# Kernel optimization log

Hardware: AMD Instinct MI355X
Metric: run time of the kernel (lower is better)

## Reference

```python
import jax, jax.numpy as jnp
import numpy as np

S, D, H, A_EMB = 128, 128, 512, 32   # memory_slots, memory_dim, integrator_hidden_dim, action_embedding_dim
FRAME_D = 512
NUM_ACTIONS = 12
T = 8192


def setup_inputs() -> dict:
    key = jax.random.key(0)
    ks = jax.random.split(key, 16)
    def rn(k, shape, scale=0.02):
        return jax.random.normal(k, shape, dtype=jnp.float32) * scale
    concat = FRAME_D + D + A_EMB
    return {
        "frame_embeds": jax.random.normal(ks[0], (T, FRAME_D), dtype=jnp.float32),
        "actions": jax.random.randint(ks[1], (T,), 0, NUM_ACTIONS),
        "action_embed_table": rn(ks[2], (NUM_ACTIONS + 1, A_EMB)),
        "W_ih": rn(ks[3], (4 * H, concat)),
        "W_hh": rn(ks[4], (4 * H, H)),
        "b_ih": jnp.zeros((4 * H,), jnp.float32),
        "b_hh": jnp.zeros((4 * H,), jnp.float32),
        "W_cls": rn(ks[5], (NUM_ACTIONS, H)),
        "b_cls": jnp.zeros((NUM_ACTIONS,), jnp.float32),
        "memory_init": rn(ks[6], (S, D)),
        "Wq": rn(ks[7], (D, H)), "bq": jnp.zeros((D,), jnp.float32),
        "Wk": rn(ks[8], (D, D)), "bk": jnp.zeros((D,), jnp.float32),
        "Wv": rn(ks[9], (D, D)), "bv": jnp.zeros((D,), jnp.float32),
        "Ww": rn(ks[10], (D, H)), "bw": jnp.zeros((D,), jnp.float32),
        "wg": rn(ks[11], (1, H)), "bg": jnp.zeros((1,), jnp.float32),
    }


def reference(frame_embeds, actions, action_embed_table, W_ih, W_hh, b_ih, b_hh,
              W_cls, b_cls, memory_init, Wq, bq, Wk, bk, Wv, bv, Ww, bw, wg, bg):
    T_ = frame_embeds.shape[0]
    # prev_actions = [start_action_index] + actions[:-1]
    prev_actions = jnp.concatenate([jnp.full((1,), NUM_ACTIONS, actions.dtype), actions[:-1]])
    prev_emb = action_embed_table[prev_actions]          # [T, A_EMB]
    keys0 = memory_init @ Wk.T + bk                      # [S, D]
    vals0 = memory_init @ Wv.T + bv                      # [S, D]
    h0 = jnp.zeros((H,), frame_embeds.dtype)
    c0 = jnp.zeros((H,), frame_embeds.dtype)
    scale = 1.0 / np.sqrt(D).astype(np.float32)

    def step(carry, xs):
        h, c, keys, vals = carry
        fe, pe, is_first = xs
        # soft memory read (skipped on step 0: retrieved = 0, and no write that step)
        q = h @ Wq.T + bq                                # [D]
        attn = jax.nn.softmax(keys @ q * scale)          # [S]
        mask = 1.0 - is_first
        retrieved = mask * (attn @ vals)                 # [D]
        x = jnp.concatenate([fe, retrieved, pe])         # [concat]
        # torch LSTMCell: gate order i, f, g, o
        gates = x @ W_ih.T + b_ih + h @ W_hh.T + b_hh    # [4H]
        i, f, g, o = jnp.split(gates, 4)
        c_new = jax.nn.sigmoid(f) * c + jax.nn.sigmoid(i) * jnp.tanh(g)
        h_new = jax.nn.sigmoid(o) * jnp.tanh(c_new)
        # gated memory write using this step's attention
        gate = jax.nn.sigmoid(h_new @ wg.T + bg)[0]      # scalar
        write_vec = h_new @ Ww.T + bw                    # [D]
        w = (mask * gate * attn)[:, None]                # [S, 1]
        vals_new = vals * (1.0 - w) + w * write_vec
        keys_new = keys * (1.0 - w) + w * write_vec
        logit = h_new @ W_cls.T + b_cls                  # [num_actions] (dropout eval = identity)
        return (h_new, c_new, keys_new, vals_new), logit

    is_first = jnp.zeros((T_,), frame_embeds.dtype).at[0].set(1.0)
    _, logits = jax.lax.scan(step, (h0, c0, keys0, vals0), (frame_embeds, prev_emb, is_first))
    return logits  # [T, num_actions]
```

## Files before the change

kernel.cpp:

```cpp
#include <hip/hip_runtime.h>

#define NGWG 128
#define TSTEPS 8192

typedef unsigned int u32;
typedef unsigned long long u64;

__device__ __forceinline__ u32 rne16(float f) {
    u32 u = __float_as_uint(f);
    return (u + 0x7fffu + ((u >> 16) & 1u)) >> 16;
}
__device__ __forceinline__ u32 packbf(float a, float b) {
    return rne16(a) | (rne16(b) << 16);
}
__device__ __forceinline__ float bflo(u32 u) { return __uint_as_float(u << 16); }
__device__ __forceinline__ float bfhi(u32 u) { return __uint_as_float(u & 0xffff0000u); }

#if __has_builtin(__builtin_amdgcn_fdot2_f32_bf16)
typedef __bf16 bf16x2 __attribute__((ext_vector_type(2)));
__device__ __forceinline__ float dot2b(u32 w, u32 h, float acc) {
    return __builtin_amdgcn_fdot2_f32_bf16(__builtin_bit_cast(bf16x2, w),
                                           __builtin_bit_cast(bf16x2, h), acc, false);
}
#else
__device__ __forceinline__ float dot2b(u32 w, u32 h, float acc) {
    return acc + bflo(w) * bflo(h) + bfhi(w) * bfhi(h);
}
#endif

__device__ __forceinline__ float rsum64(float a) {
#pragma unroll
    for (int m = 1; m < 64; m <<= 1) a += __shfl_xor(a, m);
    return a;
}
__device__ __forceinline__ float sigm(float x) { return 1.f / (1.f + __expf(-x)); }

template <typename PT>
__global__ __launch_bounds__(256) void k_pre(const float* __restrict__ fe,
                                             const int* __restrict__ act,
                                             const float* __restrict__ aet,
                                             const float* __restrict__ wih,
                                             const float* __restrict__ bih,
                                             const float* __restrict__ bhh,
                                             PT* __restrict__ P) {
    __shared__ __align__(16) float xs[32][68];
    __shared__ int pa[32];
    const int b = blockIdx.x;
    const int t0 = (b >> 3) * 32;
    const int jb = b & 7;
    const int tid = threadIdx.x;
    const int j = jb * 256 + tid;
    float acc[32];
#pragma unroll
    for (int i = 0; i < 32; i++) acc[i] = 0.f;
    if (tid < 32) {
        int t = t0 + tid;
        pa[tid] = (t == 0) ? 12 : act[t - 1];
    }
    const float* wrow = wih + (size_t)j * 672;
    for (int c = 0; c < 8; c++) {
        __syncthreads();
        for (int i = tid; i < 32 * 68; i += 256) {
            int tl = i / 68, kk = i % 68;
            int kg = c * 68 + kk;
            float v = (kg < 512) ? fe[(size_t)(t0 + tl) * 512 + kg]
                                 : aet[pa[tl] * 32 + (kg - 512)];
            xs[tl][kk] = v;
        }
        __syncthreads();
#pragma unroll
        for (int m = 0; m < 17; m++) {
            int kg0 = c * 68 + 4 * m;
            int col = (kg0 < 512) ? kg0 : kg0 + 128;
            float4 w = *(const float4*)(wrow + col);
#pragma unroll
            for (int tl = 0; tl < 32; tl++) {
                float4 x = *(const float4*)(&xs[tl][4 * m]);
                acc[tl] += w.x * x.x + w.y * x.y + w.z * x.z + w.w * x.w;
            }
        }
    }
    float bias = bih[j] + bhh[j];
    int jq = j >> 9, jrem = j & 511, jg = jrem >> 2, ju = jrem & 3;
#pragma unroll 4
    for (int tl = 0; tl < 32; tl++) {
        size_t idx = ((size_t)(t0 + tl) * NGWG + jg) * 16 + 4 * jq + ju;
        float v = acc[tl] + bias;
        if constexpr (sizeof(PT) == 2) P[idx] = (PT)rne16(v);
        else P[idx] = v;
    }
}

__global__ __launch_bounds__(256) void k_kv(const float* __restrict__ mi,
                                            const float* __restrict__ wk,
                                            const float* __restrict__ bk,
                                            const float* __restrict__ wv,
                                            const float* __restrict__ bv,
                                            float* __restrict__ kv0) {
    int o = blockIdx.x * 256 + threadIdx.x;
    int which = o >> 14;
    int rest = o & 16383;
    int s = rest >> 7, d = rest & 127;
    const float* W = which ? wv : wk;
    float acc = which ? bv[d] : bk[d];
    const float* mrow = mi + s * 128;
    const float* wrow = W + d * 128;
#pragma unroll
    for (int k = 0; k < 128; k += 4) {
        float4 a = *(const float4*)(mrow + k);
        float4 b2 = *(const float4*)(wrow + k);
        acc += a.x * b2.x + a.y * b2.y + a.z * b2.z + a.w * b2.w;
    }
    kv0[o] = acc;
}

template <typename PT>
__global__ __launch_bounds__(1024) void k_seq(const PT* __restrict__ P,
                                              const float* __restrict__ kv0,
                                              u64* __restrict__ hw,
                                              const float* __restrict__ Whh,
                                              const float* __restrict__ Wih,
                                              const float* __restrict__ Wq,
                                              const float* __restrict__ bq,
                                              const float* __restrict__ Ww,
                                              const float* __restrict__ bw,
                                              const float* __restrict__ wg,
                                              const float* __restrict__ bg,
                                              const float* __restrict__ Wcls,
                                              const float* __restrict__ bcls,
                                              float* __restrict__ out) {
    __shared__ __align__(16) float hfp[512];
    __shared__ __align__(16) u32 hbf[256];
    __shared__ __align__(16) float qwv[256];
    __shared__ float biasq[256];
    __shared__ float attn[128];
    __shared__ float warr[128];
    __shared__ float scr[128];
    __shared__ __align__(16) float part[1024];
    __shared__ float gats[16];
    __shared__ float retr[128];
    __shared__ float wgld[512];
    __shared__ float misc[4];

    const int tid = threadIdx.x;
    const int lane = tid & 63;
    const int wave = tid >> 6;
    const int g = blockIdx.x;

    if (g == NGWG) {
        float wc[8];
        float bc = 0.f;
        if (wave < 12) {
#pragma unroll
            for (int i = 0; i < 8; i++) wc[i] = Wcls[wave * 512 + 8 * lane + i];
            bc = bcls[wave];
        }
        for (int t = 0; t < TSTEPS; ++t) {
            if (tid < 512) {
                const u64* p = hw + ((size_t)((t + 1) & 3)) * 512 + tid;
                u64 v;
                do {
                    v = __hip_atomic_load(p, __ATOMIC_RELAXED, __HIP_MEMORY_SCOPE_AGENT);
                } while ((u32)(v >> 32) != (u32)(t + 1));
                hfp[tid] = __uint_as_float((u32)v);
            }
            __syncthreads();
            if (wave < 12) {
                float a = 0.f;
#pragma unroll
                for (int i = 0; i < 8; i++) a += wc[i] * hfp[8 * lane + i];
                a = rsum64(a);
                if (lane == 0) out[t * 12 + wave] = a + bc;
            }
            __syncthreads();
        }
        return;
    }

    const int seg = tid >> 8;
    const int o = tid & 255;
    const int s = tid >> 3;
    const int dc = tid & 7;
    const int dv = tid >> 3;
    const int s8 = tid & 7;

    u32 whhp[4], wirp;
    {
        int r = wave;
        int row = ((r >> 2) << 9) + 4 * g + (r & 3);
        const float* wr = Whh + (size_t)row * 512 + 8 * lane;
        float4 a = *(const float4*)wr;
        float4 b2 = *(const float4*)(wr + 4);
        whhp[0] = packbf(a.x, a.y);
        whhp[1] = packbf(a.z, a.w);
        whhp[2] = packbf(b2.x, b2.y);
        whhp[3] = packbf(b2.z, b2.w);
        const float* ir = Wih + (size_t)row * 672 + 512 + 2 * lane;
        wirp = packbf(ir[0], ir[1]);
    }
    u32 wqw[64];
    {
        const float* src = ((o < 128) ? (Wq + (size_t)o * 512) : (Ww + (size_t)(o - 128) * 512)) + seg * 128;
#pragma unroll
        for (int i = 0; i < 32; i++) {
            float4 v = *(const float4*)(src + 4 * i);
            wqw[2 * i] = packbf(v.x, v.y);
            wqw[2 * i + 1] = packbf(v.z, v.w);
        }
    }
    float keys[16], valsT[16];
    {
        const float* kp = kv0 + s * 128 + 16 * dc;
#pragma unroll
        for (int i = 0; i < 16; i++) keys[i] = kp[i];
#pragma unroll
        for (int i = 0; i < 16; i++) valsT[i] = kv0[16384 + (16 * s8 + i) * 128 + dv];
    }
    float cst = 0.f;
    const float bg0 = bg[0];

    if (tid < 512) { hfp[tid] = 0.f; wgld[tid] = wg[tid]; }
    if (tid < 256) { hbf[tid] = 0u; biasq[tid] = (tid < 128) ? bq[tid] : bw[tid - 128]; }
    if (tid < 128) { attn[tid] = 0.f; warr[tid] = 0.f; }
    if (tid < 4) misc[tid] = 0.f;
    __syncthreads();

    const float SCALE = 0.08838834764831845f;

    for (int t = 0; t < TSTEPS; ++t) {
        float pv;
        {
            size_t pidx = ((size_t)t * NGWG + g) * 16 + wave;
            if constexpr (sizeof(PT) == 2) pv = __uint_as_float(((u32)P[pidx]) << 16);
            else pv = P[pidx];
        }
        if (t > 0) {
            if (tid < 512) {
                const u64* p = hw + ((size_t)(t & 3)) * 512 + tid;
                u64 v;
                do {
                    v = __hip_atomic_load(p, __ATOMIC_RELAXED, __HIP_MEMORY_SCOPE_AGENT);
                } while ((u32)(v >> 32) != (u32)t);
                float vf = __uint_as_float((u32)v);
                hfp[tid] = vf;
                float other = __shfl_xor(vf, 1);
                if ((tid & 1) == 0) hbf[tid >> 1] = packbf(vf, other);
            }
            __syncthreads();
        }
        {
            const uint4* hb = ((const uint4*)hbf) + (seg << 4);
            float a0 = 0.f, a1 = 0.f;
#pragma unroll
            for (int i = 0; i < 16; i += 2) {
                uint4 x = hb[i];
                uint4 y = hb[i + 1];
                a0 = dot2b(wqw[4 * i + 0], x.x, a0);
                a0 = dot2b(wqw[4 * i + 1], x.y, a0);
                a0 = dot2b(wqw[4 * i + 2], x.z, a0);
                a0 = dot2b(wqw[4 * i + 3], x.w, a0);
                a1 = dot2b(wqw[4 * i + 4], y.x, a1);
                a1 = dot2b(wqw[4 * i + 5], y.y, a1);
                a1 = dot2b(wqw[4 * i + 6], y.z, a1);
                a1 = dot2b(wqw[4 * i + 7], y.w, a1);
            }
            part[tid] = a0 + a1;
        }
        if (wave == 15) {
            float a = 0.f;
#pragma unroll
            for (int i = 0; i < 8; i++) a += wgld[8 * lane + i] * hfp[8 * lane + i];
            a = rsum64(a);
            if (lane == 0) misc[0] = sigm(a + bg0);
        }
        __syncthreads();
        if (tid < 256)
            qwv[tid] = part[tid] + part[tid + 256] + part[tid + 512] + part[tid + 768] + biasq[tid];
        __syncthreads();
        {
            const float* qq = qwv + 16 * dc;
            float a = 0.f;
#pragma unroll
            for (int i = 0; i < 16; i++) a += keys[i] * qq[i];
            a += __shfl_xor(a, 1);
            a += __shfl_xor(a, 2);
            a += __shfl_xor(a, 4);
            if (dc == 0) scr[s] = a;
        }
        __syncthreads();
        if (wave == 0) {
            float a = qwv[lane] * qwv[128 + lane] + qwv[64 + lane] * qwv[192 + lane];
            float wvq = rsum64(a);
            float wmask = (t >= 2) ? 1.f : 0.f;
            float mret = (t > 0) ? 1.f : 0.f;
            float gp = misc[0];
            float w0 = wmask * gp * attn[lane];
            float w1 = wmask * gp * attn[64 + lane];
            float s0 = (scr[lane] * (1.f - w0) + w0 * wvq) * SCALE;
            float s1 = (scr[64 + lane] * (1.f - w1) + w1 * wvq) * SCALE;
            float m = fmaxf(s0, s1);
#pragma unroll
            for (int k = 1; k < 64; k <<= 1) m = fmaxf(m, __shfl_xor(m, k));
            float e0 = __expf(s0 - m), e1 = __expf(s1 - m);
            float su = rsum64(e0 + e1);
            float inv = 1.f / su;
            float a0 = e0 * inv, a1 = e1 * inv;
            attn[lane] = a0;
            attn[64 + lane] = a1;
            warr[lane] = w0;
            warr[64 + lane] = w1;
            scr[lane] = a0 * (1.f - w0) * mret;
            scr[64 + lane] = a1 * (1.f - w1) * mret;
            float bp = rsum64(a0 * w0 + a1 * w1);
            if (lane == 0) misc[2] = bp * mret;
        }
        __syncthreads();
        {
            float a = 0.f;
            const float* ap = scr + 16 * s8;
#pragma unroll
            for (int i = 0; i < 16; i++) a += ap[i] * valsT[i];
            a += __shfl_xor(a, 1);
            a += __shfl_xor(a, 2);
            a += __shfl_xor(a, 4);
            if (s8 == 0) retr[dv] = a + misc[2] * qwv[128 + dv];
        }
        __syncthreads();
        {
            const float* hh = hfp + 8 * lane;
            float a = 0.f;
#pragma unroll
            for (int i = 0; i < 4; i++) {
                u32 u = whhp[i];
                a += bflo(u) * hh[2 * i] + bfhi(u) * hh[2 * i + 1];
            }
            const float* rr = retr + 2 * lane;
            a += bflo(wirp) * rr[0] + bfhi(wirp) * rr[1];
            a = rsum64(a);
            if (lane == 0) gats[wave] = a + pv;
        }
        __syncthreads();
        if (tid < 4) {
            float gi = gats[tid], gf = gats[4 + tid], gg2 = gats[8 + tid], go = gats[12 + tid];
            cst = sigm(gf) * cst + sigm(gi) * tanhf(gg2);
            float hn = sigm(go) * tanhf(cst);
            u64 wv64 = ((u64)(u32)(t + 1) << 32) | (u64)__float_as_uint(hn);
            __hip_atomic_store(hw + ((size_t)((t + 1) & 3)) * 512 + 4 * g + tid, wv64,
                               __ATOMIC_RELAXED, __HIP_MEMORY_SCOPE_AGENT);
        }
        if (t >= 2) {
            float w = warr[s];
            const float* wvp = qwv + 128 + 16 * dc;
#pragma unroll
            for (int i = 0; i < 16; i++) keys[i] += w * (wvp[i] - keys[i]);
            float wvd = qwv[128 + dv];
#pragma unroll
            for (int i = 0; i < 16; i++) {
                float wj = warr[16 * s8 + i];
                valsT[i] += wj * (wvd - valsT[i]);
            }
        }
    }
}

extern "C" void kernel_launch(void* const* d_in, const int* in_sizes, int n_in,
                              void* d_out, int out_size, void* d_ws, size_t ws_size,
                              hipStream_t stream) {
    const float* fe = (const float*)d_in[0];
    const int* act = (const int*)d_in[1];
    const float* aet = (const float*)d_in[2];
    const float* wih = (const float*)d_in[3];
    const float* whh = (const float*)d_in[4];
    const float* bih = (const float*)d_in[5];
    const float* bhh = (const float*)d_in[6];
    const float* wcls = (const float*)d_in[7];
    const float* bcls = (const float*)d_in[8];
    const float* mi = (const float*)d_in[9];
    const float* Wq = (const float*)d_in[10];
    const float* bq = (const float*)d_in[11];
    const float* Wk = (const float*)d_in[12];
    const float* bk = (const float*)d_in[13];
    const float* Wv = (const float*)d_in[14];
    const float* bv = (const float*)d_in[15];
    const float* Ww = (const float*)d_in[16];
    const float* bw = (const float*)d_in[17];
    const float* wg = (const float*)d_in[18];
    const float* bg = (const float*)d_in[19];
    float* out = (float*)d_out;

    char* ws = (char*)d_ws;
    const size_t pfB = (size_t)TSTEPS * 2048 * 4;
    const size_t needF = pfB + 131072 + 16384;

    if (ws_size >= needF) {
        float* P = (float*)ws;
        float* kv0 = (float*)(ws + pfB);
        u64* hw = (u64*)(ws + pfB + 131072);
        k_pre<float><<<2048, 256, 0, stream>>>(fe, act, aet, wih, bih, bhh, P);
        k_kv<<<128, 256, 0, stream>>>(mi, Wk, bk, Wv, bv, kv0);
        k_seq<float><<<NGWG + 1, 1024, 0, stream>>>(P, kv0, hw, whh, wih, Wq, bq, Ww, bw,
                                                    wg, bg, wcls, bcls, out);
    } else {
        const size_t phB = (size_t)TSTEPS * 2048 * 2;
        unsigned short* P = (unsigned short*)ws;
        float* kv0 = (float*)(ws + phB);
        u64* hw = (u64*)(ws + phB + 131072);
        k_pre<unsigned short><<<2048, 256, 0, stream>>>(fe, act, aet, wih, bih, bhh, P);
        k_kv<<<128, 256, 0, stream>>>(mi, Wk, bk, Wv, bv, kv0);
        k_seq<unsigned short><<<NGWG + 1, 1024, 0, stream>>>(P, kv0, hw, whh, wih, Wq, bq,
                                                             Ww, bw, wg, bg, wcls, bcls, out);
    }
}
```

Baseline: 52.64 ms.

## Halve persistent workgroups, move classifier to post-pass, rotate register indexing

The persistent recurrent kernel now runs on 64 workgroups of 1024 threads instead of 128. Each wave computes two LSTM gate rows using fp32 weights rather than packed bf16, and the gate precompute layout is changed to match. The dedicated classifier workgroup is replaced by writing h history to the workspace and running a separate logits kernel afterward. The code also adds s_sleep to the spin-wait loops and rotates the per-thread key and value indexing to reduce LDS bank conflicts. Fewer workgroups mean cheaper cross-workgroup synchronization per step, at the cost of more per-workgroup work and extra global writes of h.

New measurement: 109.4 ms. +107.8%, slower.

```diff
diff --git a/kernel.cpp b/kernel.cpp
--- a/kernel.cpp
+++ b/kernel.cpp
@@ -1,6 +1,6 @@
 #include <hip/hip_runtime.h>
 
-#define NGWG 128
+#define NGWG 64
 #define TSTEPS 8192
 
 typedef unsigned int u32;
@@ -81,10 +81,10 @@
         }
     }
     float bias = bih[j] + bhh[j];
-    int jq = j >> 9, jrem = j & 511, jg = jrem >> 2, ju = jrem & 3;
+    int jq = j >> 9, jg = (j & 511) >> 3, jl = j & 7;
 #pragma unroll 4
     for (int tl = 0; tl < 32; tl++) {
-        size_t idx = ((size_t)(t0 + tl) * NGWG + jg) * 16 + 4 * jq + ju;
+        size_t idx = ((size_t)(t0 + tl) * NGWG + jg) * 32 + jq * 8 + jl;
         float v = acc[tl] + bias;
         if constexpr (sizeof(PT) == 2) P[idx] = (PT)rne16(v);
         else P[idx] = v;
@@ -114,10 +114,33 @@
     kv0[o] = acc;
 }
 
+__global__ __launch_bounds__(256) void k_logits(const float* __restrict__ hist,
+                                                const float* __restrict__ Wcls,
+                                                const float* __restrict__ bcls,
+                                                float* __restrict__ out) {
+    const int tid = threadIdx.x;
+    const int lane = tid & 63;
+    const int wave = tid >> 6;
+    const int t = blockIdx.x * 4 + wave;
+    const float* hrow = hist + (size_t)t * 512;
+    float hv[8];
+#pragma unroll
+    for (int i = 0; i < 8; i++) hv[i] = hrow[lane + 64 * i];
+#pragma unroll
+    for (int r = 0; r < 12; r++) {
+        float a = 0.f;
+#pragma unroll
+        for (int i = 0; i < 8; i++) a += Wcls[r * 512 + lane + 64 * i] * hv[i];
+        a = rsum64(a);
+        if (lane == 0) out[t * 12 + r] = a + bcls[r];
+    }
+}
+
 template <typename PT>
 __global__ __launch_bounds__(1024) void k_seq(const PT* __restrict__ P,
                                               const float* __restrict__ kv0,
                                               u64* __restrict__ hw,
+                                              float* __restrict__ hist,
                                               const float* __restrict__ Whh,
                                               const float* __restrict__ Wih,
                                               const float* __restrict__ Wq,
@@ -137,7 +160,7 @@
     __shared__ float warr[128];
     __shared__ float scr[128];
     __shared__ __align__(16) float part[1024];
-    __shared__ float gats[16];
+    __shared__ float gats[32];
     __shared__ float retr[128];
     __shared__ float wgld[512];
     __shared__ float misc[4];
@@ -152,23 +175,24 @@
         float bc = 0.f;
         if (wave < 12) {
 #pragma unroll
-            for (int i = 0; i < 8; i++) wc[i] = Wcls[wave * 512 + 8 * lane + i];
+            for (int i = 0; i < 8; i++) wc[i] = Wcls[wave * 512 + lane + 64 * i];
             bc = bcls[wave];
         }
         for (int t = 0; t < TSTEPS; ++t) {
             if (tid < 512) {
                 const u64* p = hw + ((size_t)((t + 1) & 3)) * 512 + tid;
-                u64 v;
-                do {
+                u64 v = __hip_atomic_load(p, __ATOMIC_RELAXED, __HIP_MEMORY_SCOPE_AGENT);
+                while ((u32)(v >> 32) != (u32)(t + 1)) {
+                    __builtin_amdgcn_s_sleep(1);
                     v = __hip_atomic_load(p, __ATOMIC_RELAXED, __HIP_MEMORY_SCOPE_AGENT);
-                } while ((u32)(v >> 32) != (u32)(t + 1));
+                }
                 hfp[tid] = __uint_as_float((u32)v);
             }
             __syncthreads();
             if (wave < 12) {
                 float a = 0.f;
 #pragma unroll
-                for (int i = 0; i < 8; i++) a += wc[i] * hfp[8 * lane + i];
+                for (int i = 0; i < 8; i++) a += wc[i] * hfp[lane + 64 * i];
                 a = rsum64(a);
                 if (lane == 0) out[t * 12 + wave] = a + bc;
             }
@@ -184,19 +208,23 @@
     const int dv = tid >> 3;
     const int s8 = tid & 7;
 
-    u32 whhp[4], wirp;
+    float whh0[8], whh1[8], wir0[2], wir1[2];
     {
-        int r = wave;
-        int row = ((r >> 2) << 9) + 4 * g + (r & 3);
-        const float* wr = Whh + (size_t)row * 512 + 8 * lane;
-        float4 a = *(const float4*)wr;
-        float4 b2 = *(const float4*)(wr + 4);
-        whhp[0] = packbf(a.x, a.y);
-        whhp[1] = packbf(a.z, a.w);
-        whhp[2] = packbf(b2.x, b2.y);
-        whhp[3] = packbf(b2.z, b2.w);
-        const float* ir = Wih + (size_t)row * 672 + 512 + 2 * lane;
-        wirp = packbf(ir[0], ir[1]);
+        const int row0 = ((wave >> 2) << 9) + 8 * g + 2 * (wave & 3);
+        const float* w0 = Whh + (size_t)row0 * 512;
+        const float* w1 = Whh + (size_t)(row0 + 1) * 512;
+#pragma unroll
+        for (int i = 0; i < 8; i++) {
+            whh0[i] = w0[lane + 64 * i];
+            whh1[i] = w1[lane + 64 * i];
+        }
+        const float* i0 = Wih + (size_t)row0 * 672 + 512;
+        const float* i1 = Wih + (size_t)(row0 + 1) * 672 + 512;
+#pragma unroll
+        for (int i = 0; i < 2; i++) {
+            wir0[i] = i0[lane + 64 * i];
+            wir1[i] = i1[lane + 64 * i];
+        }
     }
     u32 wqw[64];
     {
@@ -212,9 +240,10 @@
     {
         const float* kp = kv0 + s * 128 + 16 * dc;
 #pragma unroll
-        for (int i = 0; i < 16; i++) keys[i] = kp[i];
-#pragma unroll
-        for (int i = 0; i < 16; i++) valsT[i] = kv0[16384 + (16 * s8 + i) * 128 + dv];
+        for (int i = 0; i < 16; i++) keys[i] = kp[(i + 2 * dc) & 15];
+#pragma unroll
+        for (int i = 0; i < 16; i++)
+            valsT[i] = kv0[16384 + (16 * s8 + ((i + 2 * s8) & 15)) * 128 + dv];
     }
     float cst = 0.f;
     const float bg0 = bg[0];
@@ -228,19 +257,25 @@
     const float SCALE = 0.08838834764831845f;
 
     for (int t = 0; t < TSTEPS; ++t) {
-        float pv;
+        float pv0, pv1;
         {
-            size_t pidx = ((size_t)t * NGWG + g) * 16 + wave;
-            if constexpr (sizeof(PT) == 2) pv = __uint_as_float(((u32)P[pidx]) << 16);
-            else pv = P[pidx];
+            size_t pidx = ((size_t)t * NGWG + g) * 32 + ((wave >> 2) << 3) + 2 * (wave & 3);
+            if constexpr (sizeof(PT) == 2) {
+                pv0 = __uint_as_float(((u32)P[pidx]) << 16);
+                pv1 = __uint_as_float(((u32)P[pidx + 1]) << 16);
+            } else {
+                pv0 = P[pidx];
+                pv1 = P[pidx + 1];
+            }
         }
         if (t > 0) {
             if (tid < 512) {
                 const u64* p = hw + ((size_t)(t & 3)) * 512 + tid;
-                u64 v;
-                do {
+                u64 v = __hip_atomic_load(p, __ATOMIC_RELAXED, __HIP_MEMORY_SCOPE_AGENT);
+                while ((u32)(v >> 32) != (u32)t) {
+                    __builtin_amdgcn_s_sleep(1);
                     v = __hip_atomic_load(p, __ATOMIC_RELAXED, __HIP_MEMORY_SCOPE_AGENT);
-                } while ((u32)(v >> 32) != (u32)t);
+                }
                 float vf = __uint_as_float((u32)v);
                 hfp[tid] = vf;
                 float other = __shfl_xor(vf, 1);
@@ -269,7 +304,7 @@
         if (wave == 15) {
             float a = 0.f;
 #pragma unroll
-            for (int i = 0; i < 8; i++) a += wgld[8 * lane + i] * hfp[8 * lane + i];
+            for (int i = 0; i < 8; i++) a += wgld[lane + 64 * i] * hfp[lane + 64 * i];
             a = rsum64(a);
             if (lane == 0) misc[0] = sigm(a + bg0);
         }
@@ -281,7 +316,7 @@
             const float* qq = qwv + 16 * dc;
             float a = 0.f;
 #pragma unroll
-            for (int i = 0; i < 16; i++) a += keys[i] * qq[i];
+            for (int i = 0; i < 16; i++) a += keys[i] * qq[(i + 2 * dc) & 15];
             a += __shfl_xor(a, 1);
             a += __shfl_xor(a, 2);
             a += __shfl_xor(a, 4);
@@ -319,7 +354,7 @@
             float a = 0.f;
             const float* ap = scr + 16 * s8;
 #pragma unroll
-            for (int i = 0; i < 16; i++) a += ap[i] * valsT[i];
+            for (int i = 0; i < 16; i++) a += ap[(i + 2 * s8) & 15] * valsT[i];
             a += __shfl_xor(a, 1);
             a += __shfl_xor(a, 2);
             a += __shfl_xor(a, 4);
@@ -327,36 +362,47 @@
         }
         __syncthreads();
         {
-            const float* hh = hfp + 8 * lane;
-            float a = 0.f;
-#pragma unroll
-            for (int i = 0; i < 4; i++) {
-                u32 u = whhp[i];
-                a += bflo(u) * hh[2 * i] + bfhi(u) * hh[2 * i + 1];
-            }
-            const float* rr = retr + 2 * lane;
-            a += bflo(wirp) * rr[0] + bfhi(wirp) * rr[1];
-            a = rsum64(a);
-            if (lane == 0) gats[wave] = a + pv;
-        }
-        __syncthreads();
-        if (tid < 4) {
-            float gi = gats[tid], gf = gats[4 + tid], gg2 = gats[8 + tid], go = gats[12 + tid];
+            float a0 = 0.f, a1 = 0.f;
+#pragma unroll
+            for (int i = 0; i < 8; i++) {
+                float hv = hfp[lane + 64 * i];
+                a0 += whh0[i] * hv;
+                a1 += whh1[i] * hv;
+            }
+#pragma unroll
+            for (int i = 0; i < 2; i++) {
+                float rv = retr[lane + 64 * i];
+                a0 += wir0[i] * rv;
+                a1 += wir1[i] * rv;
+            }
+            a0 = rsum64(a0);
+            a1 = rsum64(a1);
+            if (lane == 0) {
+                int base = ((wave >> 2) << 3) + 2 * (wave & 3);
+                gats[base] = a0 + pv0;
+                gats[base + 1] = a1 + pv1;
+            }
+        }
+        __syncthreads();
+        if (tid < 8) {
+            float gi = gats[tid], gf = gats[8 + tid], gg2 = gats[16 + tid], go = gats[24 + tid];
             cst = sigm(gf) * cst + sigm(gi) * tanhf(gg2);
             float hn = sigm(go) * tanhf(cst);
             u64 wv64 = ((u64)(u32)(t + 1) << 32) | (u64)__float_as_uint(hn);
-            __hip_atomic_store(hw + ((size_t)((t + 1) & 3)) * 512 + 4 * g + tid, wv64,
+            __hip_atomic_store(hw + ((size_t)((t + 1) & 3)) * 512 + 8 * g + tid, wv64,
                                __ATOMIC_RELAXED, __HIP_MEMORY_SCOPE_AGENT);
+            if (hist) hist[(size_t)t * 512 + 8 * g + tid] = hn;
         }
         if (t >= 2) {
             float w = warr[s];
             const float* wvp = qwv + 128 + 16 * dc;
 #pragma unroll
-            for (int i = 0; i < 16; i++) keys[i] += w * (wvp[i] - keys[i]);
+            for (int i = 0; i < 16; i++) keys[i] += w * (wvp[(i + 2 * dc) & 15] - keys[i]);
             float wvd = qwv[128 + dv];
+            const float* wp = warr + 16 * s8;
 #pragma unroll
             for (int i = 0; i < 16; i++) {
-                float wj = warr[16 * s8 + i];
+                float wj = wp[(i + 2 * s8) & 15];
                 valsT[i] += wj * (wvd - valsT[i]);
             }
         }
@@ -390,24 +436,39 @@
 
     char* ws = (char*)d_ws;
     const size_t pfB = (size_t)TSTEPS * 2048 * 4;
-    const size_t needF = pfB + 131072 + 16384;
-
-    if (ws_size >= needF) {
+    const size_t kvB = 131072;
+    const size_t hwB = 4 * 512 * 8;
+    const size_t histB = (size_t)TSTEPS * 512 * 4;
+    const size_t needFull = pfB + kvB + hwB + histB;
+    const size_t needMid = pfB + kvB + hwB;
+
+    if (ws_size >= needFull) {
         float* P = (float*)ws;
         float* kv0 = (float*)(ws + pfB);
-        u64* hw = (u64*)(ws + pfB + 131072);
+        u64* hw = (u64*)(ws + pfB + kvB);
+        float* hist = (float*)(ws + pfB + kvB + hwB);
         k_pre<float><<<2048, 256, 0, stream>>>(fe, act, aet, wih, bih, bhh, P);
         k_kv<<<128, 256, 0, stream>>>(mi, Wk, bk, Wv, bv, kv0);
-        k_seq<float><<<NGWG + 1, 1024, 0, stream>>>(P, kv0, hw, whh, wih, Wq, bq, Ww, bw,
-                                                    wg, bg, wcls, bcls, out);
+        k_seq<float><<<NGWG, 1024, 0, stream>>>(P, kv0, hw, hist, whh, wih, Wq, bq, Ww, bw,
+                                                wg, bg, wcls, bcls, out);
+        k_logits<<<TSTEPS / 4, 256, 0, stream>>>(hist, wcls, bcls, out);
+    } else if (ws_size >= needMid) {
+        float* P = (float*)ws;
+        float* kv0 = (float*)(ws + pfB);
+        u64* hw = (u64*)(ws + pfB + kvB);
+        k_pre<float><<<2048, 256, 0, stream>>>(fe, act, aet, wih, bih, bhh, P);
+        k_kv<<<128, 256, 0, stream>>>(mi, Wk, bk, Wv, bv, kv0);
+        k_seq<float><<<NGWG + 1, 1024, 0, stream>>>(P, kv0, hw, (float*)nullptr, whh, wih, Wq,
+                                                    bq, Ww, bw, wg, bg, wcls, bcls, out);
     } else {
         const size_t phB = (size_t)TSTEPS * 2048 * 2;
         unsigned short* P = (unsigned short*)ws;
         float* kv0 = (float*)(ws + phB);
-        u64* hw = (u64*)(ws + phB + 131072);
+        u64* hw = (u64*)(ws + phB + kvB);
         k_pre<unsigned short><<<2048, 256, 0, stream>>>(fe, act, aet, wih, bih, bhh, P);
         k_kv<<<128, 256, 0, stream>>>(mi, Wk, bk, Wv, bv, kv0);
-        k_seq<unsigned short><<<NGWG + 1, 1024, 0, stream>>>(P, kv0, hw, whh, wih, Wq, bq,
-                                                             Ww, bw, wg, bg, wcls, bcls, out);
-    }
-}
+        k_seq<unsigned short><<<NGWG + 1, 1024, 0, stream>>>(P, kv0, hw, (float*)nullptr, whh,
+                                                             wih, Wq, bq, Ww, bw, wg, bg,
+                                                             wcls, bcls, out);
+    }
+}
```
